# Performance work log

Hardware: AMD Instinct MI355X
Metric: run time of the kernel (lower is better)

The kernel has to match this reference:

```python
import jax, jax.numpy as jnp
import numpy as np

B, C, H, W, L = 8, 32, 512, 512, 512


def setup_inputs() -> dict:
    key = jax.random.key(0)
    k1, k2, k3, k4 = jax.random.split(key, 4)
    input = jax.random.normal(k1, (B, C, H, W), dtype=jnp.float32)
    indmap = jax.random.randint(k2, (B, H, W), 0, L, dtype=jnp.int32)
    # per-bin pixel counts; >=1 so the mean-normalize never divides by zero
    output_count = jax.random.randint(k3, (B, L), 1, 1024, dtype=jnp.int32)
    valid_maps = jax.random.randint(k4, (B, H, W), 0, 2, dtype=jnp.int32)
    return {"input": input, "indmap": indmap, "output_count": output_count,
            "valid_maps": valid_maps}


def reference(input, indmap, output_count, valid_maps):
    # input: [B,C,H,W]; indmap/valid_maps: [B,H,W] (shared across C); counts: [B,L]
    x = input * valid_maps.astype(input.dtype)[:, None, :, :]          # mask-multiply
    x_flat = x.reshape(x.shape[0], x.shape[1], -1)                      # [B,C,HW]
    idx_flat = indmap.reshape(indmap.shape[0], -1)                      # [B,HW]

    def pool_one(xb, ib):
        # xb: [C,HW] -> segment_sum over pixels into L bins -> [C,L]
        return jax.ops.segment_sum(xb.T, ib, num_segments=L).T

    pooled = jax.vmap(pool_one)(x_flat, idx_flat)                       # [B,C,L]
    return pooled / output_count.astype(pooled.dtype)[:, None, :]
```

## Files before the change

### kernel.cpp

```cpp
#include <hip/hip_runtime.h>

#define B_  8
#define C_  32
#define HW_ (512 * 512)
#define L_  512

#define CG            4
#define GROUPS        (C_ / CG)
#define PIX_PER_BLOCK 8192
#define THREADS       256
#define BLOCKS_PER_B  (HW_ / PIX_PER_BLOCK)

#define SCALE_F     1048576.0f
#define INV_SCALE_F (1.0f / 1048576.0f)

typedef float f32x4 __attribute__((ext_vector_type(4)));
typedef int   i32x4 __attribute__((ext_vector_type(4)));

__global__ __launch_bounds__(THREADS, 8)
void pool_accum(const float* __restrict__ input,
                const int*   __restrict__ indmap,
                const int*   __restrict__ valid,
                unsigned*    __restrict__ wsAcc)
{
    __shared__ unsigned acc[CG * L_];

    const int bid   = blockIdx.x;
    const int b     = bid / (GROUPS * BLOCKS_PER_B);
    const int rem   = bid % (GROUPS * BLOCKS_PER_B);
    const int g     = rem / BLOCKS_PER_B;
    const int chunk = rem % BLOCKS_PER_B;
    const int t     = threadIdx.x;

    for (int i = t; i < CG * L_; i += THREADS) acc[i] = 0u;
    __syncthreads();

    const int    pbase = chunk * PIX_PER_BLOCK;
    const int*   im    = indmap + (size_t)b * HW_ + pbase;
    const int*   vm    = valid  + (size_t)b * HW_ + pbase;
    const float* inp   = input  + ((size_t)b * C_ + (size_t)g * CG) * HW_ + pbase;

    for (int it = 0; it < PIX_PER_BLOCK / (THREADS * 4); ++it) {
        const int   p0  = it * (THREADS * 4) + t * 4;
        const i32x4 idx = *reinterpret_cast<const i32x4*>(im + p0);
        const i32x4 v   = *reinterpret_cast<const i32x4*>(vm + p0);
        const float mx = v.x ? SCALE_F : 0.0f;
        const float my = v.y ? SCALE_F : 0.0f;
        const float mz = v.z ? SCALE_F : 0.0f;
        const float mw = v.w ? SCALE_F : 0.0f;

        const f32x4 x0 = __builtin_nontemporal_load(
                             reinterpret_cast<const f32x4*>(inp + 0 * (size_t)HW_ + p0));
        const f32x4 x1 = __builtin_nontemporal_load(
                             reinterpret_cast<const f32x4*>(inp + 1 * (size_t)HW_ + p0));
        const f32x4 x2 = __builtin_nontemporal_load(
                             reinterpret_cast<const f32x4*>(inp + 2 * (size_t)HW_ + p0));
        const f32x4 x3 = __builtin_nontemporal_load(
                             reinterpret_cast<const f32x4*>(inp + 3 * (size_t)HW_ + p0));

        unsigned* a0 = &acc[0 * L_];
        unsigned* a1 = &acc[1 * L_];
        unsigned* a2 = &acc[2 * L_];
        unsigned* a3 = &acc[3 * L_];

        atomicAdd(&a0[idx.x], (unsigned)__float2int_rn(x0.x * mx));
        atomicAdd(&a0[idx.y], (unsigned)__float2int_rn(x0.y * my));
        atomicAdd(&a0[idx.z], (unsigned)__float2int_rn(x0.z * mz));
        atomicAdd(&a0[idx.w], (unsigned)__float2int_rn(x0.w * mw));

        atomicAdd(&a1[idx.x], (unsigned)__float2int_rn(x1.x * mx));
        atomicAdd(&a1[idx.y], (unsigned)__float2int_rn(x1.y * my));
        atomicAdd(&a1[idx.z], (unsigned)__float2int_rn(x1.z * mz));
        atomicAdd(&a1[idx.w], (unsigned)__float2int_rn(x1.w * mw));

        atomicAdd(&a2[idx.x], (unsigned)__float2int_rn(x2.x * mx));
        atomicAdd(&a2[idx.y], (unsigned)__float2int_rn(x2.y * my));
        atomicAdd(&a2[idx.z], (unsigned)__float2int_rn(x2.z * mz));
        atomicAdd(&a2[idx.w], (unsigned)__float2int_rn(x2.w * mw));

        atomicAdd(&a3[idx.x], (unsigned)__float2int_rn(x3.x * mx));
        atomicAdd(&a3[idx.y], (unsigned)__float2int_rn(x3.y * my));
        atomicAdd(&a3[idx.z], (unsigned)__float2int_rn(x3.z * mz));
        atomicAdd(&a3[idx.w], (unsigned)__float2int_rn(x3.w * mw));
    }
    __syncthreads();

    unsigned* wb = wsAcc + ((size_t)b * C_ + (size_t)g * CG) * L_;
    for (int e = t; e < CG * L_; e += THREADS)
        atomicAdd(&wb[e], acc[e]);
}

__global__ __launch_bounds__(256)
void pool_finalize(const int* __restrict__ wsAcc,
                   const int* __restrict__ out_count,
                   float*     __restrict__ out)
{
    const int e = blockIdx.x * 256 + threadIdx.x;
    const int b = e / (C_ * L_);
    const int l = e & (L_ - 1);
    out[e] = (float)wsAcc[e] * INV_SCALE_F / (float)out_count[b * L_ + l];
}

extern "C" void kernel_launch(void* const* d_in, const int* in_sizes, int n_in,
                              void* d_out, int out_size, void* d_ws, size_t ws_size,
                              hipStream_t stream) {
    const float* input     = (const float*)d_in[0];
    const int*   indmap    = (const int*)  d_in[1];
    const int*   out_count = (const int*)  d_in[2];
    const int*   valid     = (const int*)  d_in[3];
    float*       out       = (float*)      d_out;

    unsigned* wsAcc = (unsigned*)d_ws;
    (void)hipMemsetAsync(wsAcc, 0, (size_t)B_ * C_ * L_ * sizeof(int), stream);

    const dim3 grid(B_ * GROUPS * BLOCKS_PER_B);
    pool_accum<<<grid, THREADS, 0, stream>>>(input, indmap, valid, wsAcc);
    pool_finalize<<<(B_ * C_ * L_) / 256, 256, 0, stream>>>((const int*)wsAcc,
                                                            out_count, out);
}
```

Measured before the change: 58.65 us.

## Fuse finalize into accumulation kernel via float atomic adds to output

Removes the separate finalize kernel: each block scales its fixed-point shared-memory partials by the inverse scale and per-bin count, then atomically adds floats straight into the output, which is zeroed by a memset. This saves one kernel launch and the workspace round trip. The price is nondeterministic float atomic summation order across the 32 chunk blocks. It also drops the nontemporal hint on the input loads.

```diff
diff --git a/kernel.cpp b/kernel.cpp
--- a/kernel.cpp
+++ b/kernel.cpp
@@ -20,8 +20,9 @@
 __global__ __launch_bounds__(THREADS, 8)
 void pool_accum(const float* __restrict__ input,
                 const int*   __restrict__ indmap,
+                const int*   __restrict__ out_count,
                 const int*   __restrict__ valid,
-                unsigned*    __restrict__ wsAcc)
+                float*       __restrict__ out)
 {
     __shared__ unsigned acc[CG * L_];
 
@@ -49,14 +50,10 @@
         const float mz = v.z ? SCALE_F : 0.0f;
         const float mw = v.w ? SCALE_F : 0.0f;
 
-        const f32x4 x0 = __builtin_nontemporal_load(
-                             reinterpret_cast<const f32x4*>(inp + 0 * (size_t)HW_ + p0));
-        const f32x4 x1 = __builtin_nontemporal_load(
-                             reinterpret_cast<const f32x4*>(inp + 1 * (size_t)HW_ + p0));
-        const f32x4 x2 = __builtin_nontemporal_load(
-                             reinterpret_cast<const f32x4*>(inp + 2 * (size_t)HW_ + p0));
-        const f32x4 x3 = __builtin_nontemporal_load(
-                             reinterpret_cast<const f32x4*>(inp + 3 * (size_t)HW_ + p0));
+        const f32x4 x0 = *reinterpret_cast<const f32x4*>(inp + 0 * (size_t)HW_ + p0);
+        const f32x4 x1 = *reinterpret_cast<const f32x4*>(inp + 1 * (size_t)HW_ + p0);
+        const f32x4 x2 = *reinterpret_cast<const f32x4*>(inp + 2 * (size_t)HW_ + p0);
+        const f32x4 x3 = *reinterpret_cast<const f32x4*>(inp + 3 * (size_t)HW_ + p0);
 
         unsigned* a0 = &acc[0 * L_];
         unsigned* a1 = &acc[1 * L_];
@@ -85,20 +82,12 @@
     }
     __syncthreads();
 
-    unsigned* wb = wsAcc + ((size_t)b * C_ + (size_t)g * CG) * L_;
-    for (int e = t; e < CG * L_; e += THREADS)
-        atomicAdd(&wb[e], acc[e]);
-}
-
-__global__ __launch_bounds__(256)
-void pool_finalize(const int* __restrict__ wsAcc,
-                   const int* __restrict__ out_count,
-                   float*     __restrict__ out)
-{
-    const int e = blockIdx.x * 256 + threadIdx.x;
-    const int b = e / (C_ * L_);
-    const int l = e & (L_ - 1);
-    out[e] = (float)wsAcc[e] * INV_SCALE_F / (float)out_count[b * L_ + l];
+    const int* cnt = out_count + (size_t)b * L_;
+    float*     ob  = out + ((size_t)b * C_ + (size_t)g * CG) * L_;
+    for (int e = t; e < CG * L_; e += THREADS) {
+        const int l = e & (L_ - 1);
+        unsafeAtomicAdd(&ob[e], (float)(int)acc[e] * INV_SCALE_F / (float)cnt[l]);
+    }
 }
 
 extern "C" void kernel_launch(void* const* d_in, const int* in_sizes, int n_in,
@@ -110,11 +99,8 @@
     const int*   valid     = (const int*)  d_in[3];
     float*       out       = (float*)      d_out;
 
-    unsigned* wsAcc = (unsigned*)d_ws;
-    (void)hipMemsetAsync(wsAcc, 0, (size_t)B_ * C_ * L_ * sizeof(int), stream);
+    (void)hipMemsetAsync(out, 0, (size_t)out_size * sizeof(float), stream);
 
     const dim3 grid(B_ * GROUPS * BLOCKS_PER_B);
-    pool_accum<<<grid, THREADS, 0, stream>>>(input, indmap, valid, wsAcc);
-    pool_finalize<<<(B_ * C_ * L_) / 256, 256, 0, stream>>>((const int*)wsAcc,
-                                                            out_count, out);
+    pool_accum<<<grid, THREADS, 0, stream>>>(input, indmap, out_count, valid, out);
 }
```

Result: faster. 56.94 us (-2.9%).
